# Performance work log

Measured on AMD Instinct MI355X. Metric: run time of the kernel, lower is better.

Reference implementation:

```python
import jax, jax.numpy as jnp
import numpy as np

S = 4   # stride
NH = 4  # n_heads
NP = 4  # n_points


def conv2d(x, w, b, pad):
    out = jax.lax.conv_general_dilated(x, w, (1, 1), [(pad, pad), (pad, pad)],
                                       dimension_numbers=('NCHW', 'OIHW', 'NCHW'))
    return out + b[None, :, None, None]


def leaky(x):
    return jnp.where(x >= 0, x, 0.1 * x)


def seq_net(x, w0, b0, w1, b1, w2, b2, w3, b3):
    x = leaky(conv2d(x, w0, b0, 0))
    x = leaky(conv2d(x, w1, b1, 1))
    x = leaky(conv2d(x, w2, b2, 1))
    return conv2d(x, w3, b3, 0)


def fold_s(x, C, hs, ws):
    # inverse of unfold(kernel=S, stride=S): (N, C*S*S, hs*ws) -> (N, C, hs*S, ws*S)
    N = x.shape[0]
    x = x.reshape(N, C, S, S, hs, ws)
    return x.transpose(0, 1, 4, 2, 5, 3).reshape(N, C, hs * S, ws * S)


def unfold_s(x):
    # (N, C, h, w) -> (N, C*S*S, h//S, w//S), kernel=S, stride=S
    N, C, h, w = x.shape
    hs, ws = h // S, w // S
    x = x.reshape(N, C, hs, S, ws, S).transpose(0, 1, 3, 5, 2, 4)
    return x.reshape(N, C * S * S, hs, ws)


def avgpool_s(x):
    # adaptive_avg_pool2d (h,w)->(h/S,w/S) == mean over SxS blocks
    N, C, h, w = x.shape
    return x.reshape(N, C, h // S, S, w // S, S).mean(axis=(3, 5))


def grid_sample_nearest(img, grid):
    # img (N,C,H,W); grid (N,A,B,2) normalized; nearest, zeros padding, align_corners=True
    N, C, H, W = img.shape
    ix = jnp.round((grid[..., 0] + 1.0) * 0.5 * (W - 1))
    iy = jnp.round((grid[..., 1] + 1.0) * 0.5 * (H - 1))
    valid = (ix >= 0) & (ix <= W - 1) & (iy >= 0) & (iy <= H - 1)
    ixi = jnp.clip(ix, 0, W - 1).astype(jnp.int32)
    iyi = jnp.clip(iy, 0, H - 1).astype(jnp.int32)
    out = jax.vmap(lambda im, yy, xx: im[:, yy, xx])(img, iyi, ixi)  # (N,C,A,B)
    return out * valid[:, None].astype(img.dtype)


def ltff_forward(anchor_feat, sparse_feat_set_s1, flow_buffers,
                 so_w0, so_b0, so_w1, so_b1, so_w2, so_b2, so_w3, so_b3,
                 aw_w0, aw_b0, aw_w1, aw_b1, aw_w2, aw_b2, aw_w3, aw_b3,
                 fusion_w, fusion_b):
    n, c, h, w = anchor_feat.shape
    t = sparse_feat_set_s1.shape[1]
    hs, ws = h // S, w // S
    ch = c // NH  # per-head channels

    gy, gx = jnp.meshgrid(jnp.arange(hs), jnp.arange(ws), indexing='ij')
    loc_ref = jnp.stack([gx, gy], 0).astype(flow_buffers.dtype)[None, None]  # (1,1,2,hs,ws)
    location_feat = flow_buffers + loc_ref  # (n,t,2,hs,ws)

    # flow-warp the (strided) sparse feature set; align_corners=True norm uses dim-1
    gf = location_feat.transpose(0, 1, 3, 4, 2)  # (n,t,hs,ws,2)
    gfx = 2.0 * gf[..., 0] / max(ws - 1, 1) - 1.0
    gfy = 2.0 * gf[..., 1] / max(hs - 1, 1) - 1.0
    grid1 = jnp.stack([gfx, gfy], -1).reshape(n * t, hs, ws, 2)

    sp = sparse_feat_set_s1.reshape(n * t, c * S * S, hs, ws)
    warp = grid_sample_nearest(sp, grid1)
    out_res = fold_s(warp.reshape(n * t, c * S * S, hs * ws), c, hs, ws)  # (n*t,c,h,w)
    out_ori = fold_s(sp.reshape(n * t, c * S * S, hs * ws), c, hs, ws)

    extra = jnp.concatenate([avgpool_s(out_ori), avgpool_s(out_res),
                             flow_buffers.reshape(n * t, 2, hs, ws)], axis=1)  # (n*t,2c+2,hs,ws)

    offsets = seq_net(extra, so_w0, so_b0, so_w1, so_b1, so_w2, so_b2, so_w3, so_b3)
    offsets = offsets.reshape(n * t, NH * NP, 2, hs, ws)
    attn = seq_net(extra, aw_w0, aw_b0, aw_w1, aw_b1, aw_w2, aw_b2, aw_w3, aw_b3)
    attn = (attn.reshape(n, t, NH, NP, hs, ws)
                .transpose(0, 2, 4, 5, 1, 3)
                .reshape(n * NH, hs, ws, t * NP))
    attn = jax.nn.softmax(attn, axis=-1)

    og = location_feat.reshape(n * t, 1, 2, hs, ws) + offsets  # (n*t, NH*NP, 2, hs, ws)
    og = og.transpose(0, 1, 3, 4, 2)
    ogx = 2.0 * og[..., 0] / ws - 1.0  # original divides by dim (not dim-1) here
    ogy = 2.0 * og[..., 1] / hs - 1.0
    og = jnp.stack([ogx, ogy], -1).reshape(n, t, NH, NP, hs * ws, 2)
    og = og.transpose(0, 1, 2, 4, 3, 5).reshape(n * t * NH, hs * ws, NP, 2)

    vals = out_ori.reshape(n * t * NH, ch, h, w)
    vals = unfold_s(vals)  # (n*t*NH, ch*S*S, hs, ws)
    sampled = grid_sample_nearest(vals, og)  # (n*t*NH, ch*S*S, hs*ws, NP)
    sampled = (sampled.reshape(n, t, NH, ch * S * S, hs, ws, NP)
                      .transpose(0, 2, 3, 4, 5, 1, 6)
                      .reshape(n * NH, ch * S * S, hs, ws, t * NP))

    out = (sampled * attn[:, None]).sum(-1)  # (n*NH, ch*S*S, hs, ws)
    out = fold_s(out.reshape(n * NH, ch * S * S, hs * ws), ch, hs, ws).reshape(n, c, h, w)
    out = conv2d(out, fusion_w, fusion_b, 1) + anchor_feat
    return out


def setup_inputs():
    key = jax.random.key(0)
    ks = jax.random.split(key, 16)
    n, t, c, h, w = 2, 3, 128, 192, 192
    hs, ws = h // S, w // S
    cin = 2 * c + 2  # 258
    m = 64
    f32 = jnp.float32
    def rn(k, shape, scale=1.0):
        return jax.random.normal(k, shape, dtype=f32) * scale
    return {
        'curr_feat': rn(ks[0], (n, c, h, w)),
        'anchor_feat': rn(ks[1], (n, c, h, w)),
        'sparse_feat_set_s1': rn(ks[2], (n, t, c * S * S, hs, ws)),
        'flow_buffers': rn(ks[3], (n, t, 2, hs, ws)),
        'so_w0': rn(ks[4], (m, cin, 1, 1), 0.05), 'so_b0': jnp.zeros((m,), f32),
        'so_w1': rn(ks[5], (m, m, 3, 3), 0.05), 'so_b1': jnp.zeros((m,), f32),
        'so_w2': rn(ks[6], (m, m, 3, 3), 0.05), 'so_b2': jnp.zeros((m,), f32),
        'so_w3': rn(ks[7], (NH * NP * 2, m, 1, 1), 0.05), 'so_b3': jnp.zeros((NH * NP * 2,), f32),
        'aw_w0': rn(ks[8], (m, cin, 1, 1), 0.05), 'aw_b0': jnp.zeros((m,), f32),
        'aw_w1': rn(ks[9], (m, m, 3, 3), 0.05), 'aw_b1': jnp.zeros((m,), f32),
        'aw_w2': rn(ks[10], (m, m, 3, 3), 0.05), 'aw_b2': jnp.zeros((m,), f32),
        'aw_w3': rn(ks[11], (NH * NP, m, 1, 1), 0.05), 'aw_b3': jnp.zeros((NH * NP,), f32),
        'fusion_w': rn(ks[12], (c, c, 3, 3), 0.02), 'fusion_b': jnp.zeros((c,), f32),
    }


def reference(curr_feat, anchor_feat, sparse_feat_set_s1, flow_buffers,
              so_w0, so_b0, so_w1, so_b1, so_w2, so_b2, so_w3, so_b3,
              aw_w0, aw_b0, aw_w1, aw_b1, aw_w2, aw_b2, aw_w3, aw_b3,
              fusion_w, fusion_b):
    # curr_feat is accepted by the original forward but never used
    return ltff_forward(anchor_feat, sparse_feat_set_s1, flow_buffers,
                        so_w0, so_b0, so_w1, so_b1, so_w2, so_b2, so_w3, so_b3,
                        aw_w0, aw_b0, aw_w1, aw_b1, aw_w2, aw_b2, aw_w3, aw_b3,
                        fusion_w, fusion_b)
```

## Files before the change

kernel.cpp:

```cpp
#include <hip/hip_runtime.h>

typedef unsigned short u16;
typedef unsigned int u32;
typedef __attribute__((ext_vector_type(8))) short bf16x8;
typedef __attribute__((ext_vector_type(4))) float f32x4;

#define HS   48
#define WSB  48
#define NPIX 2304
#define CCH  128
#define NT   6
#define CIN  258
#define HH   192
#define WW   192

#define EXTRA_OFF  0ull
#define OUTIMG_OFF 0ull
#define XA_OFF     4718592ull
#define XB_OFF     6488064ull
#define OFFS_OFF   8257536ull
#define ARAW_OFF   8699904ull
#define WT_OFF     8921088ull
#define SPT_OFF    4718592ull
#define ATTNW_OFF  11796480ull
#define SIDX_OFF   12017664ull
#define WBF_OFF    12238848ull

#define SPT2_OFF    0ull
#define EXTRA2_OFF  14155776ull
#define OUTIMG2_OFF 14155776ull
#define XA2_OFF     17722368ull
#define XB2_OFF     19491840ull
#define OFFS2_OFF   21261312ull
#define ARAW2_OFF   21703680ull
#define WT2_OFF     21924864ull
#define ATTNW2_OFF  22072320ull
#define SIDX2_OFF   22293504ull
#define WBF2_OFF    22514688ull
#define TOTAL2_F32  22588416ull

static __device__ __forceinline__ float leaky_f(float v) { return v >= 0.f ? v : 0.1f * v; }
static __device__ __forceinline__ u16 f2bf(float f) {
    u32 u = __float_as_uint(f);
    u = (u + 0x7fffu + ((u >> 16) & 1u)) >> 16;
    return (u16)u;
}
static __device__ __forceinline__ float bf2f(u16 v) {
    u32 u = ((u32)v) << 16;
    return __uint_as_float(u);
}

__global__ __launch_bounds__(256) void k_wprep(const float* __restrict__ fw, u16* __restrict__ wbf) {
    int i = blockIdx.x * 256 + threadIdx.x;
    int j  = i & 7;
    int g  = (i >> 3) & 3;
    int oc = (i >> 5) & 127;
    int kcd = i >> 12;
    int d = kcd >> 2, kc = kcd & 3;
    int ic = kc * 32 + g * 8 + j;
    wbf[i] = f2bf(fw[((size_t)oc * 128 + ic) * 9 + d]);
}

__global__ __launch_bounds__(256) void k_wprep2(const float* __restrict__ so_w1, const float* __restrict__ aw_w1,
                                                const float* __restrict__ so_w2, const float* __restrict__ aw_w2,
                                                float* __restrict__ wT) {
    int i = blockIdx.x * 256 + threadIdx.x;
    int l   = i / 73728;
    int r1  = i % 73728;
    int net = r1 / 36864;
    int r   = r1 % 36864;
    int ic  = r / 576;
    int t2  = r % 576;
    int tap = t2 >> 6, oc = t2 & 63;
    const float* src = l ? (net ? aw_w2 : so_w2) : (net ? aw_w1 : so_w1);
    wT[i] = src[(size_t)oc * 576 + ic * 9 + tap];
}

__global__ __launch_bounds__(256) void k_avgpool(const float* __restrict__ sp,
                                                 float* __restrict__ extra) {
    int idx = blockIdx.x * 256 + threadIdx.x;
    if (idx >= NT * CCH * NPIX) return;
    int pix = idx % NPIX;
    int cc  = (idx / NPIX) % CCH;
    int nt  = idx / (NPIX * CCH);
    const float* p = sp + ((size_t)nt * 2048 + (size_t)cc * 16) * NPIX + pix;
    float s = 0.f;
#pragma unroll
    for (int k = 0; k < 16; k++) s += p[(size_t)k * NPIX];
    extra[((size_t)nt * CIN + cc) * NPIX + pix] = s * 0.0625f;
}

__global__ __launch_bounds__(256) void k_spprep(const float* __restrict__ sp,
                                                u16* __restrict__ spT2,
                                                float* __restrict__ extra) {
    __shared__ float tile[64][65];
    int tid = threadIdx.x;
    int pix0 = blockIdx.x * 64;
    int ch0  = blockIdx.y * 64;
    int nt   = blockIdx.z;
    const float* base = sp + ((size_t)nt * 2048 + ch0) * NPIX + pix0;
#pragma unroll
    for (int k = 0; k < 16; k++) {
        int row = k * 4 + (tid >> 6);
        int col = tid & 63;
        tile[row][col] = base[(size_t)row * NPIX + col];
    }
    __syncthreads();
#pragma unroll
    for (int k = 0; k < 2; k++) {
        int task = k * 256 + tid;
        int pl = task >> 3;
        int c0 = (task & 7) * 8;
        u16 pk[8];
#pragma unroll
        for (int j = 0; j < 8; j++) pk[j] = f2bf(tile[c0 + j][pl]);
        *reinterpret_cast<int4*>(spT2 + ((size_t)nt * NPIX + pix0 + pl) * 2048 + ch0 + c0) =
            *reinterpret_cast<const int4*>(pk);
    }
    {
        int ccl = tid >> 6;
        int col = tid & 63;
        float s = 0.f;
#pragma unroll
        for (int k = 0; k < 16; k++) s += tile[ccl * 16 + k][col];
        int cc = (ch0 >> 4) + ccl;
        extra[((size_t)nt * CIN + cc) * NPIX + pix0 + col] = s * 0.0625f;
    }
}

__global__ __launch_bounds__(256) void k_extra_rest(const float* __restrict__ flow,
                                                    float* __restrict__ extra) {
    int idx = blockIdx.x * 256 + threadIdx.x;
    if (idx >= NT * 130 * NPIX) return;
    int pix = idx % NPIX;
    int cc  = (idx / NPIX) % 130;
    int nt  = idx / (NPIX * 130);
    float fx = flow[((size_t)nt * 2 + 0) * NPIX + pix];
    float fy = flow[((size_t)nt * 2 + 1) * NPIX + pix];
    if (cc >= 128) {
        extra[((size_t)nt * CIN + 256 + (cc - 128)) * NPIX + pix] = (cc == 128) ? fx : fy;
        return;
    }
    int x = pix % WSB, y = pix / WSB;
    float locx = fx + (float)x;
    float locy = fy + (float)y;
    float gfx = 2.0f * locx / 47.0f - 1.0f;
    float gfy = 2.0f * locy / 47.0f - 1.0f;
    float rx = rintf(((gfx + 1.0f) * 0.5f) * 47.0f);
    float ry = rintf(((gfy + 1.0f) * 0.5f) * 47.0f);
    bool valid = (rx >= 0.f) && (rx <= 47.f) && (ry >= 0.f) && (ry <= 47.f);
    int sx = (int)fminf(fmaxf(rx, 0.f), 47.f);
    int sy = (int)fminf(fmaxf(ry, 0.f), 47.f);
    float v = valid ? extra[((size_t)nt * CIN + cc) * NPIX + sy * WSB + sx] : 0.f;
    extra[((size_t)nt * CIN + 128 + cc) * NPIX + pix] = v;
}

__global__ __launch_bounds__(256) void k_conv1x1_l0(const float* __restrict__ extra,
                                                    const float* __restrict__ w_so, const float* __restrict__ b_so,
                                                    const float* __restrict__ w_aw, const float* __restrict__ b_aw,
                                                    float* __restrict__ xa) {
    __shared__ float ws_[16 * CIN];
    int tile = blockIdx.x;
    int nt   = blockIdx.y;
    int z    = blockIdx.z;
    int net = z >> 2, ocg = z & 3;
    const float* wsel = net ? w_aw : w_so;
    const float* bsel = net ? b_aw : b_so;
    for (int i = threadIdx.x; i < 16 * CIN; i += 256)
        ws_[i] = wsel[(size_t)(ocg * 16) * CIN + i];
    __syncthreads();
    int pix = tile * 256 + threadIdx.x;
    float acc[16];
#pragma unroll
    for (int o = 0; o < 16; o++) acc[o] = bsel[ocg * 16 + o];
    const float* in = extra + (size_t)nt * CIN * NPIX + pix;
    for (int ci = 0; ci < CIN; ci++) {
        float v = in[(size_t)ci * NPIX];
#pragma unroll
        for (int o = 0; o < 16; o++) acc[o] = fmaf(ws_[o * CIN + ci], v, acc[o]);
    }
    float* op = xa + (((size_t)net * NT + nt) * 64 + ocg * 16) * NPIX + pix;
#pragma unroll
    for (int o = 0; o < 16; o++) op[(size_t)o * NPIX] = leaky_f(acc[o]);
}

__global__ __launch_bounds__(256) void k_conv3x3(const float* __restrict__ xin,
                                                 const float* __restrict__ wT,
                                                 const float* __restrict__ b_so, const float* __restrict__ b_aw,
                                                 float* __restrict__ xout) {
    __shared__ float At[16][6][24];
    __shared__ float Bt[16][9][64];
    int tid = threadIdx.x;
    int txq = tid & 3, tyq = (tid >> 2) & 3, ocg = tid >> 4;
    int st = blockIdx.x;
    int x0 = (st % 3) * 16, y0 = (st / 3) * 4;
    int nt = blockIdx.y, net = blockIdx.z;
    const float* in  = xin + ((size_t)net * NT + nt) * 64 * NPIX;
    const float* wTn = wT + (size_t)net * 36864;
    const float* bsel = net ? b_aw : b_so;

    float acc[4][4];
#pragma unroll
    for (int o = 0; o < 4; o++) {
        float bv = bsel[ocg * 4 + o];
#pragma unroll
        for (int p = 0; p < 4; p++) acc[o][p] = bv;
    }

    for (int c0 = 0; c0 < 64; c0 += 16) {
        __syncthreads();
        for (int i = tid; i < 1728; i += 256) {
            int ic = i / 108, r = i % 108;
            int ry = r / 18, rx = r % 18;
            int gy = y0 + ry - 1, gx = x0 + rx - 1;
            float v = 0.f;
            if (gy >= 0 && gy < HS && gx >= 0 && gx < WSB)
                v = in[(size_t)(c0 + ic) * NPIX + gy * WSB + gx];
            At[ic][ry][rx] = v;
        }
        {
            const float* src = wTn + (size_t)c0 * 576;
            float* dst = &Bt[0][0][0];
            for (int i = tid; i < 9216; i += 256) dst[i] = src[i];
        }
        __syncthreads();
#pragma unroll 2
        for (int ic = 0; ic < 16; ic++) {
#pragma unroll
            for (int dy = 0; dy < 3; dy++) {
                f32x4 a0 = *reinterpret_cast<const f32x4*>(&At[ic][tyq + dy][4 * txq]);
                f32x4 a1 = *reinterpret_cast<const f32x4*>(&At[ic][tyq + dy][4 * txq + 4]);
#pragma unroll
                for (int dx = 0; dx < 3; dx++) {
                    f32x4 bv = *reinterpret_cast<const f32x4*>(&Bt[ic][dy * 3 + dx][4 * ocg]);
#pragma unroll
                    for (int p = 0; p < 4; p++) {
                        float av = (dx + p < 4) ? a0[dx + p] : a1[dx + p - 4];
#pragma unroll
                        for (int o = 0; o < 4; o++)
                            acc[o][p] = fmaf(bv[o], av, acc[o][p]);
                    }
                }
            }
        }
    }

    int py = y0 + tyq, pxb = x0 + 4 * txq;
#pragma unroll
    for (int o = 0; o < 4; o++) {
        f32x4 res;
#pragma unroll
        for (int p = 0; p < 4; p++) res[p] = leaky_f(acc[o][p]);
        float* op = xout + (((size_t)net * NT + nt) * 64 + ocg * 4 + o) * NPIX + py * WSB + pxb;
        *reinterpret_cast<f32x4*>(op) = res;
    }
}

__global__ __launch_bounds__(256) void k_conv1x1_l3(const float* __restrict__ xin,
                                                    const float* __restrict__ w_so, const float* __restrict__ b_so,
                                                    const float* __restrict__ w_aw, const float* __restrict__ b_aw,
                                                    float* __restrict__ offs, float* __restrict__ araw) {
    int pix = blockIdx.x * 256 + threadIdx.x;
    int nt = blockIdx.y;
    int net = blockIdx.z;
    const float* in = xin + ((size_t)net * NT + nt) * 64 * NPIX + pix;
    if (net == 0) {
        float acc[32];
#pragma unroll
        for (int o = 0; o < 32; o++) acc[o] = b_so[o];
        for (int ci = 0; ci < 64; ci++) {
            float v = in[(size_t)ci * NPIX];
#pragma unroll
            for (int o = 0; o < 32; o++) acc[o] = fmaf(w_so[o * 64 + ci], v, acc[o]);
        }
#pragma unroll
        for (int o = 0; o < 32; o++) offs[((size_t)nt * 32 + o) * NPIX + pix] = acc[o];
    } else {
        float acc[16];
#pragma unroll
        for (int o = 0; o < 16; o++) acc[o] = b_aw[o];
        for (int ci = 0; ci < 64; ci++) {
            float v = in[(size_t)ci * NPIX];
#pragma unroll
            for (int o = 0; o < 16; o++) acc[o] = fmaf(w_aw[o * 64 + ci], v, acc[o]);
        }
#pragma unroll
        for (int o = 0; o < 16; o++) araw[((size_t)nt * 16 + o) * NPIX + pix] = acc[o];
    }
}

__global__ __launch_bounds__(256) void k_softmax_idx(const float* __restrict__ araw,
                                                     const float* __restrict__ offs,
                                                     const float* __restrict__ flow,
                                                     float* __restrict__ attnw, int* __restrict__ sidx) {
    int idx = blockIdx.x * 256 + threadIdx.x;
    if (idx >= 2 * 4 * NPIX) return;
    int pix  = idx % NPIX;
    int head = (idx / NPIX) & 3;
    int n    = idx / (NPIX * 4);
    int x = pix % WSB, y = pix / WSB;
    float a[12];
#pragma unroll
    for (int t = 0; t < 3; t++)
#pragma unroll
        for (int p = 0; p < 4; p++)
            a[t * 4 + p] = araw[(((size_t)(n * 3 + t)) * 16 + head * 4 + p) * NPIX + pix];
    float mx = a[0];
#pragma unroll
    for (int k = 1; k < 12; k++) mx = fmaxf(mx, a[k]);
    float ssum = 0.f;
#pragma unroll
    for (int k = 0; k < 12; k++) { a[k] = expf(a[k] - mx); ssum += a[k]; }
    float inv = 1.0f / ssum;
#pragma unroll
    for (int t = 0; t < 3; t++) {
        int nt = n * 3 + t;
        float fx = flow[((size_t)nt * 2 + 0) * NPIX + pix];
        float fy = flow[((size_t)nt * 2 + 1) * NPIX + pix];
        float locx = fx + (float)x;
        float locy = fy + (float)y;
#pragma unroll
        for (int p = 0; p < 4; p++) {
            int hp = head * 4 + p;
            float gx_ = locx + offs[(((size_t)nt) * 32 + hp * 2 + 0) * NPIX + pix];
            float gy_ = locy + offs[(((size_t)nt) * 32 + hp * 2 + 1) * NPIX + pix];
            float ngx = 2.0f * gx_ / 48.0f - 1.0f;
            float ngy = 2.0f * gy_ / 48.0f - 1.0f;
            float rx = rintf(((ngx + 1.0f) * 0.5f) * 47.0f);
            float ry = rintf(((ngy + 1.0f) * 0.5f) * 47.0f);
            bool valid = (rx >= 0.f) && (rx <= 47.f) && (ry >= 0.f) && (ry <= 47.f);
            int sx = (int)fminf(fmaxf(rx, 0.f), 47.f);
            int sy = (int)fminf(fmaxf(ry, 0.f), 47.f);
            int k = t * 4 + p;
            attnw[(size_t)idx * 12 + k] = valid ? a[k] * inv : 0.f;
            sidx[(size_t)idx * 12 + k]  = sy * WSB + sx;
        }
    }
}

__global__ __launch_bounds__(256) void k_transpose(const float* __restrict__ sp,
                                                   u16* __restrict__ spT, int n) {
    __shared__ float tile[64][65];
    int tid = threadIdx.x;
    int pix0 = blockIdx.x * 64;
    int ch0  = blockIdx.y * 64;
    int tl   = blockIdx.z;
    int nt = n * 3 + tl;
    const float* base = sp + ((size_t)nt * 2048 + ch0) * NPIX + pix0;
#pragma unroll
    for (int k = 0; k < 16; k++) {
        int row = k * 4 + (tid >> 6);
        int col = tid & 63;
        tile[row][col] = base[(size_t)row * NPIX + col];
    }
    __syncthreads();
#pragma unroll
    for (int k = 0; k < 2; k++) {
        int task = k * 256 + tid;
        int pl = task >> 3;
        int c0 = (task & 7) * 8;
        u16 pk[8];
#pragma unroll
        for (int j = 0; j < 8; j++) pk[j] = f2bf(tile[c0 + j][pl]);
        *reinterpret_cast<int4*>(spT + ((size_t)tl * NPIX + pix0 + pl) * 2048 + ch0 + c0) =
            *reinterpret_cast<const int4*>(pk);
    }
}

__global__ __launch_bounds__(256) void k_gather2(const u16* __restrict__ spT,
                                                 const float* __restrict__ attnw,
                                                 const int* __restrict__ sidx,
                                                 u16* __restrict__ outimg, int n) {
    __shared__ u16 sArr[2048 + 128];
    int tid = threadIdx.x;
    int pix = blockIdx.x;
    int y = pix / WSB, x = pix % WSB;
    int h = tid >> 6;
    int lane = tid & 63;
    size_t ab = ((size_t)(n * 4 + h) * NPIX + pix) * 12;
    float acc[8] = {};
#pragma unroll
    for (int t = 0; t < 3; t++) {
#pragma unroll
        for (int p = 0; p < 4; p++) {
            int k = t * 4 + p;
            float w = attnw[ab + k];
            int idx = sidx[ab + k];
            bf16x8 v = *reinterpret_cast<const bf16x8*>(
                spT + ((size_t)t * NPIX + idx) * 2048 + h * 512 + lane * 8);
#pragma unroll
            for (int j = 0; j < 8; j++)
                acc[j] = fmaf(w, bf2f((u16)v[j]), acc[j]);
        }
    }
    int c0 = h * 512 + lane * 8;
    int si = c0 + (c0 >> 4);
    u16 pk[8];
#pragma unroll
    for (int j = 0; j < 8; j++) pk[j] = f2bf(acc[j]);
    *reinterpret_cast<int4*>(&sArr[si]) = *reinterpret_cast<const int4*>(pk);
    __syncthreads();
    int opix = tid >> 4;
    int oc0 = (tid & 15) * 8;
    u16 ov[8];
#pragma unroll
    for (int j = 0; j < 8; j++) {
        int oc = oc0 + j;
        int ch = (oc >> 5) * 512 + (oc & 31) * 16 + opix;
        ov[j] = sArr[ch + (ch >> 4)];
    }
    int hq = y * 4 + (opix >> 2);
    int wq = x * 4 + (opix & 3);
    *reinterpret_cast<int4*>(outimg + (((size_t)(n * HH + hq) * WW + wq) << 7) + oc0) =
        *reinterpret_cast<const int4*>(ov);
}

__global__ __launch_bounds__(256, 3) void k_fusion_mfma(const u16* __restrict__ img,
                                                        const u16* __restrict__ wbf,
                                                        const float* __restrict__ bias,
                                                        const float* __restrict__ anchor,
                                                        float* __restrict__ out) {
    __shared__ __align__(16) u16 lds_in[180 * 128];

    const int tid = threadIdx.x;
    const int px0 = blockIdx.x * 16;
    const int py0 = blockIdx.y * 8;
    const int nb  = blockIdx.z >> 1;
    const int ocq = blockIdx.z & 1;
    const int lane = tid & 63;
    const int w = tid >> 6;
    const int r = lane & 15, g = lane >> 4;

    char* lin_b = reinterpret_cast<char*>(lds_in);

    for (int i = tid; i < 180 * 16; i += 256) {
        int p = i >> 4, c16 = i & 15;
        int hy = p / 18, hx = p % 18;
        int gy = py0 + hy - 1, gx = px0 + hx - 1;
        int4 v = make_int4(0, 0, 0, 0);
        if (gy >= 0 && gy < HH && gx >= 0 && gx < WW)
            v = *reinterpret_cast<const int4*>(img + (((size_t)(nb * HH + gy) * WW + gx) << 7) + (c16 << 3));
        *reinterpret_cast<int4*>(lin_b + p * 256 + (((c16 ^ (p & 7)) << 4))) = v;
    }

    const u16* wb = wbf + (size_t)(ocq * 64 + r) * 32 + g * 8;

    f32x4 acc[2][4] = {};
    bf16x8 b[2][4];
#pragma unroll
    for (int n = 0; n < 4; n++)
        b[0][n] = *reinterpret_cast<const bf16x8*>(wb + (size_t)n * 512);

    __syncthreads();

#pragma unroll
    for (int ph = 0; ph < 36; ph++) {
        const int d = ph >> 2, kc = ph & 3;
        const int dy = d / 3, dx = d % 3;
        if (ph < 35) {
#pragma unroll
            for (int n = 0; n < 4; n++)
                b[(ph + 1) & 1][n] = *reinterpret_cast<const bf16x8*>(
                    wb + (size_t)(ph + 1) * 4096 + (size_t)n * 512);
        }
        const int c16 = kc * 4 + g;
        bf16x8 a[2];
#pragma unroll
        for (int m = 0; m < 2; m++) {
            int hp = (2 * w + m + dy) * 18 + (r + dx);
            a[m] = *reinterpret_cast<const bf16x8*>(lin_b + hp * 256 + (((c16 ^ (hp & 7)) << 4)));
        }
#pragma unroll
        for (int m = 0; m < 2; m++)
#pragma unroll
            for (int n = 0; n < 4; n++)
                acc[m][n] = __builtin_amdgcn_mfma_f32_16x16x32_bf16(a[m], b[ph & 1][n], acc[m][n], 0, 0, 0);
    }

    float bs[4];
#pragma unroll
    for (int n = 0; n < 4; n++) bs[n] = bias[ocq * 64 + n * 16 + r];
#pragma unroll
    for (int m = 0; m < 2; m++) {
        int gy = py0 + 2 * w + m;
#pragma unroll
        for (int n = 0; n < 4; n++) {
            int oc = ocq * 64 + n * 16 + r;
            size_t oa = ((size_t)(nb * CCH + oc)) * (HH * WW) + (size_t)gy * WW + px0 + g * 4;
            f32x4 av = *reinterpret_cast<const f32x4*>(anchor + oa);
            f32x4 res;
#pragma unroll
            for (int q = 0; q < 4; q++) res[q] = acc[m][n][q] + bs[n] + av[q];
            *reinterpret_cast<f32x4*>(out + oa) = res;
        }
    }
}

extern "C" void kernel_launch(void* const* d_in, const int* in_sizes, int n_in,
                              void* d_out, int out_size, void* d_ws, size_t ws_size,
                              hipStream_t stream) {
    (void)in_sizes; (void)n_in; (void)out_size;
    const float* anchor = (const float*)d_in[1];
    const float* sp     = (const float*)d_in[2];
    const float* flow   = (const float*)d_in[3];
    const float* so_w0 = (const float*)d_in[4];  const float* so_b0 = (const float*)d_in[5];
    const float* so_w1 = (const float*)d_in[6];  const float* so_b1 = (const float*)d_in[7];
    const float* so_w2 = (const float*)d_in[8];  const float* so_b2 = (const float*)d_in[9];
    const float* so_w3 = (const float*)d_in[10]; const float* so_b3 = (const float*)d_in[11];
    const float* aw_w0 = (const float*)d_in[12]; const float* aw_b0 = (const float*)d_in[13];
    const float* aw_w1 = (const float*)d_in[14]; const float* aw_b1 = (const float*)d_in[15];
    const float* aw_w2 = (const float*)d_in[16]; const float* aw_b2 = (const float*)d_in[17];
    const float* aw_w3 = (const float*)d_in[18]; const float* aw_b3 = (const float*)d_in[19];
    const float* fw    = (const float*)d_in[20]; const float* fb    = (const float*)d_in[21];

    float* ws   = (float*)d_ws;
    float* outp = (float*)d_out;
    const bool big = ws_size >= TOTAL2_F32 * 4ull;

    float* extra; float* xa; float* xb; float* offs; float* araw; float* wT;
    float* attnw; int* sidx; u16* wbf; u16* outimg;

    if (big) {
        extra = ws + EXTRA2_OFF;  xa = ws + XA2_OFF;    xb = ws + XB2_OFF;
        offs  = ws + OFFS2_OFF;   araw = ws + ARAW2_OFF; wT = ws + WT2_OFF;
        attnw = ws + ATTNW2_OFF;  sidx = (int*)(ws + SIDX2_OFF);
        wbf   = (u16*)(ws + WBF2_OFF);  outimg = (u16*)(ws + OUTIMG2_OFF);
    } else {
        extra = ws + EXTRA_OFF;   xa = ws + XA_OFF;     xb = ws + XB_OFF;
        offs  = ws + OFFS_OFF;    araw = ws + ARAW_OFF;  wT = ws + WT_OFF;
        attnw = ws + ATTNW_OFF;   sidx = (int*)(ws + SIDX_OFF);
        wbf   = (u16*)(ws + WBF_OFF);   outimg = (u16*)(ws + OUTIMG_OFF);
    }

    k_wprep<<<dim3(576), 256, 0, stream>>>(fw, wbf);
    k_wprep2<<<dim3(576), 256, 0, stream>>>(so_w1, aw_w1, so_w2, aw_w2, wT);

    if (big) {
        u16* spT2 = (u16*)(ws + SPT2_OFF);
        k_spprep<<<dim3(36, 32, 6), 256, 0, stream>>>(sp, spT2, extra);
        k_extra_rest<<<dim3((NT * 130 * NPIX + 255) / 256), 256, 0, stream>>>(flow, extra);
        k_conv1x1_l0<<<dim3(9, 6, 8), 256, 0, stream>>>(extra, so_w0, so_b0, aw_w0, aw_b0, xa);
        k_conv3x3<<<dim3(36, 6, 2), 256, 0, stream>>>(xa, wT, so_b1, aw_b1, xb);
        k_conv3x3<<<dim3(36, 6, 2), 256, 0, stream>>>(xb, wT + 73728, so_b2, aw_b2, xa);
        k_conv1x1_l3<<<dim3(9, 6, 2), 256, 0, stream>>>(xa, so_w3, so_b3, aw_w3, aw_b3, offs, araw);
        k_softmax_idx<<<dim3((2 * 4 * NPIX + 255) / 256), 256, 0, stream>>>(araw, offs, flow, attnw, sidx);
        for (int n = 0; n < 2; n++)
            k_gather2<<<dim3(NPIX), 256, 0, stream>>>(spT2 + (size_t)n * 3 * NPIX * 2048,
                                                      attnw, sidx, outimg, n);
    } else {
        u16* spT = (u16*)(ws + SPT_OFF);
        k_avgpool<<<dim3((NT * CCH * NPIX + 255) / 256), 256, 0, stream>>>(sp, extra);
        k_extra_rest<<<dim3((NT * 130 * NPIX + 255) / 256), 256, 0, stream>>>(flow, extra);
        k_conv1x1_l0<<<dim3(9, 6, 8), 256, 0, stream>>>(extra, so_w0, so_b0, aw_w0, aw_b0, xa);
        k_conv3x3<<<dim3(36, 6, 2), 256, 0, stream>>>(xa, wT, so_b1, aw_b1, xb);
        k_conv3x3<<<dim3(36, 6, 2), 256, 0, stream>>>(xb, wT + 73728, so_b2, aw_b2, xa);
        k_conv1x1_l3<<<dim3(9, 6, 2), 256, 0, stream>>>(xa, so_w3, so_b3, aw_w3, aw_b3, offs, araw);
        k_softmax_idx<<<dim3((2 * 4 * NPIX + 255) / 256), 256, 0, stream>>>(araw, offs, flow, attnw, sidx);
        for (int n = 0; n < 2; n++) {
            k_transpose<<<dim3(36, 32, 3), 256, 0, stream>>>(sp, spT, n);
            k_gather2<<<dim3(NPIX), 256, 0, stream>>>(spT, attnw, sidx, outimg, n);
        }
    }
    k_fusion_mfma<<<dim3(WW / 16, HH / 8, 4), 256, 0, stream>>>(outimg, wbf, fb, anchor, outp);
}
```

Baseline: 281.4 us.

## Write gathered image into zero-padded buffer and fuse conv without LDS staging

The gather kernel now writes its output into a zero-padded (194x194) NHWC bf16 image, cleared beforehand with a memset. A new fusion conv kernel reads MFMA operands directly from that padded buffer in global memory, so it needs no LDS tile, halo handling or barriers. It also uses a different tile shape (32x4 pixels) and higher occupancy. In exchange it pays for an extra memset, and more redundant global loads now rely on the cache. Only the large-workspace path changes.

```diff
diff --git a/kernel.cpp b/kernel.cpp
--- a/kernel.cpp
+++ b/kernel.cpp
@@ -13,6 +13,7 @@
 #define CIN  258
 #define HH   192
 #define WW   192
+#define PW   194
 
 #define EXTRA_OFF  0ull
 #define OUTIMG_OFF 0ull
@@ -28,7 +29,7 @@
 
 #define SPT2_OFF    0ull
 #define EXTRA2_OFF  14155776ull
-#define OUTIMG2_OFF 14155776ull
+#define IMGP_OFF    14155776ull
 #define XA2_OFF     17722368ull
 #define XB2_OFF     19491840ull
 #define OFFS2_OFF   21261312ull
@@ -415,6 +416,54 @@
         *reinterpret_cast<const int4*>(ov);
 }
 
+__global__ __launch_bounds__(256) void k_gather2p(const u16* __restrict__ spT,
+                                                  const float* __restrict__ attnw,
+                                                  const int* __restrict__ sidx,
+                                                  u16* __restrict__ imgP, int n) {
+    __shared__ u16 sArr[2048 + 128];
+    int tid = threadIdx.x;
+    int pix = blockIdx.x;
+    int y = pix / WSB, x = pix % WSB;
+    int h = tid >> 6;
+    int lane = tid & 63;
+    size_t ab = ((size_t)(n * 4 + h) * NPIX + pix) * 12;
+    float acc[8] = {};
+#pragma unroll
+    for (int t = 0; t < 3; t++) {
+#pragma unroll
+        for (int p = 0; p < 4; p++) {
+            int k = t * 4 + p;
+            float w = attnw[ab + k];
+            int idx = sidx[ab + k];
+            bf16x8 v = *reinterpret_cast<const bf16x8*>(
+                spT + ((size_t)t * NPIX + idx) * 2048 + h * 512 + lane * 8);
+#pragma unroll
+            for (int j = 0; j < 8; j++)
+                acc[j] = fmaf(w, bf2f((u16)v[j]), acc[j]);
+        }
+    }
+    int c0 = h * 512 + lane * 8;
+    int si = c0 + (c0 >> 4);
+    u16 pk[8];
+#pragma unroll
+    for (int j = 0; j < 8; j++) pk[j] = f2bf(acc[j]);
+    *reinterpret_cast<int4*>(&sArr[si]) = *reinterpret_cast<const int4*>(pk);
+    __syncthreads();
+    int opix = tid >> 4;
+    int oc0 = (tid & 15) * 8;
+    u16 ov[8];
+#pragma unroll
+    for (int j = 0; j < 8; j++) {
+        int oc = oc0 + j;
+        int ch = (oc >> 5) * 512 + (oc & 31) * 16 + opix;
+        ov[j] = sArr[ch + (ch >> 4)];
+    }
+    int hq = y * 4 + (opix >> 2);
+    int wq = x * 4 + (opix & 3);
+    *reinterpret_cast<int4*>(imgP + (((size_t)(n * PW + hq + 1) * PW + wq + 1) << 7) + oc0) =
+        *reinterpret_cast<const int4*>(ov);
+}
+
 __global__ __launch_bounds__(256, 3) void k_fusion_mfma(const u16* __restrict__ img,
                                                         const u16* __restrict__ wbf,
                                                         const float* __restrict__ bias,
@@ -487,6 +536,74 @@
         for (int n = 0; n < 4; n++) {
             int oc = ocq * 64 + n * 16 + r;
             size_t oa = ((size_t)(nb * CCH + oc)) * (HH * WW) + (size_t)gy * WW + px0 + g * 4;
+            f32x4 av = *reinterpret_cast<const f32x4*>(anchor + oa);
+            f32x4 res;
+#pragma unroll
+            for (int q = 0; q < 4; q++) res[q] = acc[m][n][q] + bs[n] + av[q];
+            *reinterpret_cast<f32x4*>(out + oa) = res;
+        }
+    }
+}
+
+__global__ __launch_bounds__(256, 4) void k_fusion_direct(const u16* __restrict__ imgP,
+                                                          const u16* __restrict__ wbf,
+                                                          const float* __restrict__ bias,
+                                                          const float* __restrict__ anchor,
+                                                          float* __restrict__ out) {
+    const int tid = threadIdx.x;
+    const int px0 = blockIdx.x * 32;
+    const int py0 = blockIdx.y * 4;
+    const int nb  = blockIdx.z >> 1;
+    const int ocq = blockIdx.z & 1;
+    const int lane = tid & 63;
+    const int w = tid >> 6;
+    const int r = lane & 15, g = lane >> 4;
+
+    const u16* ia = imgP + (((size_t)(nb * PW + py0 + w) * PW + px0 + r) << 7) + g * 8;
+    const u16* wb = wbf + (size_t)(ocq * 64 + r) * 32 + g * 8;
+
+    f32x4 acc[2][4] = {};
+    bf16x8 b[2][4], a[2][2];
+#pragma unroll
+    for (int n = 0; n < 4; n++)
+        b[0][n] = *reinterpret_cast<const bf16x8*>(wb + (size_t)n * 512);
+#pragma unroll
+    for (int m = 0; m < 2; m++)
+        a[0][m] = *reinterpret_cast<const bf16x8*>(ia + ((size_t)(m * 16) << 7));
+
+#pragma unroll
+    for (int ph = 0; ph < 36; ph++) {
+        if (ph < 35) {
+            const int ph1 = ph + 1;
+            const int d1 = ph1 >> 2, kc1 = ph1 & 3;
+            const int dy1 = d1 / 3, dx1 = d1 % 3;
+#pragma unroll
+            for (int n = 0; n < 4; n++)
+                b[ph1 & 1][n] = *reinterpret_cast<const bf16x8*>(
+                    wb + (size_t)ph1 * 4096 + (size_t)n * 512);
+#pragma unroll
+            for (int m = 0; m < 2; m++)
+                a[ph1 & 1][m] = *reinterpret_cast<const bf16x8*>(
+                    ia + ((size_t)(dy1 * PW + m * 16 + dx1) << 7) + kc1 * 32);
+        }
+#pragma unroll
+        for (int m = 0; m < 2; m++)
+#pragma unroll
+            for (int n = 0; n < 4; n++)
+                acc[m][n] = __builtin_amdgcn_mfma_f32_16x16x32_bf16(a[ph & 1][m], b[ph & 1][n], acc[m][n], 0, 0, 0);
+    }
+
+    float bs[4];
+#pragma unroll
+    for (int n = 0; n < 4; n++) bs[n] = bias[ocq * 64 + n * 16 + r];
+    const int gy = py0 + w;
+#pragma unroll
+    for (int n = 0; n < 4; n++) {
+        int oc = ocq * 64 + n * 16 + r;
+        size_t rowb = ((size_t)(nb * CCH + oc)) * (HH * WW) + (size_t)gy * WW + px0 + g * 4;
+#pragma unroll
+        for (int m = 0; m < 2; m++) {
+            size_t oa = rowb + m * 16;
             f32x4 av = *reinterpret_cast<const f32x4*>(anchor + oa);
             f32x4 res;
 #pragma unroll
@@ -517,26 +634,21 @@
     float* outp = (float*)d_out;
     const bool big = ws_size >= TOTAL2_F32 * 4ull;
 
-    float* extra; float* xa; float* xb; float* offs; float* araw; float* wT;
-    float* attnw; int* sidx; u16* wbf; u16* outimg;
-
     if (big) {
-        extra = ws + EXTRA2_OFF;  xa = ws + XA2_OFF;    xb = ws + XB2_OFF;
-        offs  = ws + OFFS2_OFF;   araw = ws + ARAW2_OFF; wT = ws + WT2_OFF;
-        attnw = ws + ATTNW2_OFF;  sidx = (int*)(ws + SIDX2_OFF);
-        wbf   = (u16*)(ws + WBF2_OFF);  outimg = (u16*)(ws + OUTIMG2_OFF);
-    } else {
-        extra = ws + EXTRA_OFF;   xa = ws + XA_OFF;     xb = ws + XB_OFF;
-        offs  = ws + OFFS_OFF;    araw = ws + ARAW_OFF;  wT = ws + WT_OFF;
-        attnw = ws + ATTNW_OFF;   sidx = (int*)(ws + SIDX_OFF);
-        wbf   = (u16*)(ws + WBF_OFF);   outimg = (u16*)(ws + OUTIMG_OFF);
-    }
-
-    k_wprep<<<dim3(576), 256, 0, stream>>>(fw, wbf);
-    k_wprep2<<<dim3(576), 256, 0, stream>>>(so_w1, aw_w1, so_w2, aw_w2, wT);
-
-    if (big) {
-        u16* spT2 = (u16*)(ws + SPT2_OFF);
+        float* extra = ws + EXTRA2_OFF;
+        float* xa    = ws + XA2_OFF;
+        float* xb    = ws + XB2_OFF;
+        float* offs  = ws + OFFS2_OFF;
+        float* araw  = ws + ARAW2_OFF;
+        float* wT    = ws + WT2_OFF;
+        float* attnw = ws + ATTNW2_OFF;
+        int*   sidx  = (int*)(ws + SIDX2_OFF);
+        u16*   wbf   = (u16*)(ws + WBF2_OFF);
+        u16*   spT2  = (u16*)(ws + SPT2_OFF);
+        u16*   imgP  = (u16*)(ws + IMGP_OFF);
+
+        k_wprep<<<dim3(576), 256, 0, stream>>>(fw, wbf);
+        k_wprep2<<<dim3(576), 256, 0, stream>>>(so_w1, aw_w1, so_w2, aw_w2, wT);
         k_spprep<<<dim3(36, 32, 6), 256, 0, stream>>>(sp, spT2, extra);
         k_extra_rest<<<dim3((NT * 130 * NPIX + 255) / 256), 256, 0, stream>>>(flow, extra);
         k_conv1x1_l0<<<dim3(9, 6, 8), 256, 0, stream>>>(extra, so_w0, so_b0, aw_w0, aw_b0, xa);
@@ -544,11 +656,26 @@
         k_conv3x3<<<dim3(36, 6, 2), 256, 0, stream>>>(xb, wT + 73728, so_b2, aw_b2, xa);
         k_conv1x1_l3<<<dim3(9, 6, 2), 256, 0, stream>>>(xa, so_w3, so_b3, aw_w3, aw_b3, offs, araw);
         k_softmax_idx<<<dim3((2 * 4 * NPIX + 255) / 256), 256, 0, stream>>>(araw, offs, flow, attnw, sidx);
+        hipMemsetAsync(imgP, 0, (size_t)2 * PW * PW * 128 * sizeof(u16), stream);
         for (int n = 0; n < 2; n++)
-            k_gather2<<<dim3(NPIX), 256, 0, stream>>>(spT2 + (size_t)n * 3 * NPIX * 2048,
-                                                      attnw, sidx, outimg, n);
+            k_gather2p<<<dim3(NPIX), 256, 0, stream>>>(spT2 + (size_t)n * 3 * NPIX * 2048,
+                                                       attnw, sidx, imgP, n);
+        k_fusion_direct<<<dim3(WW / 32, HH / 4, 4), 256, 0, stream>>>(imgP, wbf, fb, anchor, outp);
     } else {
-        u16* spT = (u16*)(ws + SPT_OFF);
+        float* extra = ws + EXTRA_OFF;
+        float* xa    = ws + XA_OFF;
+        float* xb    = ws + XB_OFF;
+        float* offs  = ws + OFFS_OFF;
+        float* araw  = ws + ARAW_OFF;
+        float* wT    = ws + WT_OFF;
+        float* attnw = ws + ATTNW_OFF;
+        int*   sidx  = (int*)(ws + SIDX_OFF);
+        u16*   wbf   = (u16*)(ws + WBF_OFF);
+        u16*   outimg = (u16*)(ws + OUTIMG_OFF);
+        u16*   spT   = (u16*)(ws + SPT_OFF);
+
+        k_wprep<<<dim3(576), 256, 0, stream>>>(fw, wbf);
+        k_wprep2<<<dim3(576), 256, 0, stream>>>(so_w1, aw_w1, so_w2, aw_w2, wT);
         k_avgpool<<<dim3((NT * CCH * NPIX + 255) / 256), 256, 0, stream>>>(sp, extra);
         k_extra_rest<<<dim3((NT * 130 * NPIX + 255) / 256), 256, 0, stream>>>(flow, extra);
         k_conv1x1_l0<<<dim3(9, 6, 8), 256, 0, stream>>>(extra, so_w0, so_b0, aw_w0, aw_b0, xa);
@@ -560,6 +687,6 @@
             k_transpose<<<dim3(36, 32, 3), 256, 0, stream>>>(sp, spT, n);
             k_gather2<<<dim3(NPIX), 256, 0, stream>>>(spT, attnw, sidx, outimg, n);
         }
-    }
-    k_fusion_mfma<<<dim3(WW / 16, HH / 8, 4), 256, 0, stream>>>(outimg, wbf, fb, anchor, outp);
-}
+        k_fusion_mfma<<<dim3(WW / 16, HH / 8, 4), 256, 0, stream>>>(outimg, wbf, fb, anchor, outp);
+    }
+}
```

Result: slower. 322.1 us (+14.5%).
